# Optimization experiments

Hardware: AMD Instinct MI355X
Metric: run time of the kernel (lower is better)

## Reference

```python
import jax, jax.numpy as jnp
import numpy as np

TEMPERATURE = 0.02
EPS = 1e-10
TOPK = 10


def setup_inputs() -> dict:
    key = jax.random.key(0)
    k1, k2 = jax.random.split(key)
    B = 8192
    sim_matrix = jax.random.normal(k1, (B, B), dtype=jnp.float32)
    pids = jax.random.randint(k2, (B,), 0, 1000, dtype=jnp.int64)
    return {"sim_matrix": sim_matrix, "pids": pids}


def reference(sim_matrix, pids):
    B = sim_matrix.shape[0]
    k = min(TOPK, B)

    # Entropy of the T->I matching distribution per row (matches torch exactly:
    # softmax over dim=1, then -sum p*log(p+eps)).
    probs = jax.nn.softmax(sim_matrix / TEMPERATURE, axis=1)  # [B, B]
    entropy = -jnp.sum(probs * jnp.log(probs + EPS), axis=1)  # [B]
    max_entropy = np.float32(np.log(B + EPS))
    normalized_entropy = entropy / max_entropy  # [B]

    # Vectorized top-k rank agreement between T->I rows and I->T rows
    # (replaces the original per-sample Python loop with set intersection;
    # top-k indices are unique, so counting pairwise equality == |set A & set B|).
    _, top_t2i = jax.lax.top_k(sim_matrix, k)      # [B, k]
    _, top_i2t = jax.lax.top_k(sim_matrix.T, k)    # [B, k]
    overlap = jnp.sum(
        top_t2i[:, :, None] == top_i2t[:, None, :], axis=(1, 2)
    )  # [B]
    rank_agreement = overlap.astype(sim_matrix.dtype) / k  # [B]

    uncertainty = (1.0 - rank_agreement) * 0.5 + normalized_entropy * 0.5
    return uncertainty, normalized_entropy
```

## Files before the change

### kernel.cpp

```cpp
#include <hip/hip_runtime.h>
#include <hip/hip_bf16.h>
#include <math.h>

constexpr int BB = 8192;
constexpr float INV_MAX_ENT = 1.0f / 9.010913347279288f;

#define CAS_STEP(tvk, tik)                                  \
  if (_cv > tvk) {                                          \
    float _fv = tvk; tvk = _cv; _cv = _fv;                  \
    int _fi = tik; tik = _ci; _ci = _fi;                    \
  }

#define INS10(vv, ii)                                       \
  if ((vv) > tv9) {                                         \
    float _cv = (vv);                                       \
    int _ci = (ii);                                         \
    CAS_STEP(tv0, ti0) CAS_STEP(tv1, ti1)                   \
    CAS_STEP(tv2, ti2) CAS_STEP(tv3, ti3)                   \
    CAS_STEP(tv4, ti4) CAS_STEP(tv5, ti5)                   \
    CAS_STEP(tv6, ti6) CAS_STEP(tv7, ti7)                   \
    CAS_STEP(tv8, ti8) CAS_STEP(tv9, ti9)                   \
  }

#define DECL10                                              \
  float tv0 = -INFINITY, tv1 = -INFINITY, tv2 = -INFINITY,  \
        tv3 = -INFINITY, tv4 = -INFINITY, tv5 = -INFINITY,  \
        tv6 = -INFINITY, tv7 = -INFINITY, tv8 = -INFINITY,  \
        tv9 = -INFINITY;                                    \
  int ti0 = -1, ti1 = -1, ti2 = -1, ti3 = -1, ti4 = -1,     \
      ti5 = -1, ti6 = -1, ti7 = -1, ti8 = -1, ti9 = -1;

#define POP_HEAD                                            \
  tv0 = tv1; ti0 = ti1; tv1 = tv2; ti1 = ti2;               \
  tv2 = tv3; ti2 = ti3; tv3 = tv4; ti3 = ti4;               \
  tv4 = tv5; ti4 = ti5; tv5 = tv6; ti5 = ti6;               \
  tv6 = tv7; ti6 = ti7; tv7 = tv8; ti7 = ti8;               \
  tv8 = tv9; ti8 = ti9; tv9 = -INFINITY; ti9 = -1;

__global__ __launch_bounds__(256) void rows_kernel(const float* __restrict__ sim,
                                                   float* __restrict__ out,
                                                   int* __restrict__ row_top) {
  const int lane = threadIdx.x & 63;
  const int wid = threadIdx.x >> 6;
  const int row = blockIdx.x * 4 + wid;

  const float4* __restrict__ r4 =
      reinterpret_cast<const float4*>(sim + (size_t)row * BB);

  DECL10;
  float m = -1e30f, S = 0.0f, W = 0.0f;

#pragma unroll 4
  for (int j4 = 0; j4 < 32; ++j4) {
    const int f = lane + (j4 << 6);
    float4 q = r4[f];

    float mx4 = fmaxf(fmaxf(q.x, q.y), fmaxf(q.z, q.w));
    if (mx4 > tv9) {
      const int base = f << 2;
      INS10(q.x, base + 0);
      INS10(q.y, base + 1);
      INS10(q.z, base + 2);
      INS10(q.w, base + 3);
    }

    float t0 = 50.0f * q.x, t1 = 50.0f * q.y, t2 = 50.0f * q.z, t3 = 50.0f * q.w;
    float bm = fmaxf(fmaxf(t0, t1), fmaxf(t2, t3));
    float mn = fmaxf(m, bm);
    float r = __expf(m - mn);
    float d0 = t0 - mn, d1 = t1 - mn, d2 = t2 - mn, d3 = t3 - mn;
    float e0 = __expf(d0), e1 = __expf(d1), e2 = __expf(d2), e3 = __expf(d3);
    W = fmaf(m - mn, S, W) * r + (d0 * e0 + d1 * e1 + d2 * e2 + d3 * e3);
    S = fmaf(S, r, (e0 + e1) + (e2 + e3));
    m = mn;
  }

#pragma unroll
  for (int off = 32; off; off >>= 1) {
    float m2 = __shfl_xor(m, off);
    float S2 = __shfl_xor(S, off);
    float W2 = __shfl_xor(W, off);
    float mn = fmaxf(m, m2);
    float ra = __expf(m - mn);
    float rb = __expf(m2 - mn);
    W = fmaf(m - mn, S, W) * ra + fmaf(m2 - mn, S2, W2) * rb;
    S = S * ra + S2 * rb;
    m = mn;
  }
  if (lane == 0) {
    out[BB + row] = (__logf(S) - W / S) * INV_MAX_ENT;
  }

#pragma unroll 1
  for (int kk = 0; kk < 10; ++kk) {
    float v = tv0;
    int i = ti0;
#pragma unroll
    for (int off = 32; off; off >>= 1) {
      float ov = __shfl_xor(v, off);
      int oi = __shfl_xor(i, off);
      if (ov > v || (ov == v && oi < i)) { v = ov; i = oi; }
    }
    if (lane == 0) row_top[kk * BB + row] = i;
    if (ti0 == i) { POP_HEAD }
  }
}

__global__ __launch_bounds__(256) void cols_partial_kernel(const float* __restrict__ sim,
                                                           float* __restrict__ pv,
                                                           int* __restrict__ pi,
                                                           int CH) {
  const int col = blockIdx.x * 256 + threadIdx.x;
  const int r0 = blockIdx.y * CH;

  DECL10;

  const float* __restrict__ p = sim + (size_t)r0 * BB + col;

  for (int rr = 0; rr < CH; rr += 8) {
    float v0 = p[0 * BB];
    float v1 = p[1 * BB];
    float v2 = p[2 * BB];
    float v3 = p[3 * BB];
    float v4 = p[4 * BB];
    float v5 = p[5 * BB];
    float v6 = p[6 * BB];
    float v7 = p[7 * BB];
    p += (size_t)8 * BB;
    float mx = fmaxf(fmaxf(fmaxf(v0, v1), fmaxf(v2, v3)),
                     fmaxf(fmaxf(v4, v5), fmaxf(v6, v7)));
    if (mx > tv9) {
      INS10(v0, r0 + rr + 0);
      INS10(v1, r0 + rr + 1);
      INS10(v2, r0 + rr + 2);
      INS10(v3, r0 + rr + 3);
      INS10(v4, r0 + rr + 4);
      INS10(v5, r0 + rr + 5);
      INS10(v6, r0 + rr + 6);
      INS10(v7, r0 + rr + 7);
    }
  }

  float* __restrict__ pvb = pv + (size_t)blockIdx.y * 10 * BB + col;
  int* __restrict__ pib = pi + (size_t)blockIdx.y * 10 * BB + col;
  pvb[0 * BB] = tv0;  pib[0 * BB] = ti0;
  pvb[1 * BB] = tv1;  pib[1 * BB] = ti1;
  pvb[2 * BB] = tv2;  pib[2 * BB] = ti2;
  pvb[3 * BB] = tv3;  pib[3 * BB] = ti3;
  pvb[4 * BB] = tv4;  pib[4 * BB] = ti4;
  pvb[5 * BB] = tv5;  pib[5 * BB] = ti5;
  pvb[6 * BB] = tv6;  pib[6 * BB] = ti6;
  pvb[7 * BB] = tv7;  pib[7 * BB] = ti7;
  pvb[8 * BB] = tv8;  pib[8 * BB] = ti8;
  pvb[9 * BB] = tv9;  pib[9 * BB] = ti9;
}

__global__ __launch_bounds__(256) void merge_kernel(const float* __restrict__ pv,
                                                    const int* __restrict__ pi,
                                                    const int* __restrict__ row_top,
                                                    float* __restrict__ out,
                                                    int nch) {
  const int c = blockIdx.x * 256 + threadIdx.x;

  DECL10;

  for (int ch = 0; ch < nch; ++ch) {
    const float* __restrict__ pvb = pv + (size_t)ch * 10 * BB + c;
    const int* __restrict__ pib = pi + (size_t)ch * 10 * BB + c;
#pragma unroll
    for (int j = 0; j < 10; ++j) {
      float vj = pvb[j * BB];
      if (!(vj > tv9)) break;
      int idj = pib[j * BB];
      INS10(vj, idj);
    }
  }

  int cnt = 0;
#pragma unroll
  for (int kk = 0; kk < 10; ++kk) {
    int rt = row_top[kk * BB + c];
    cnt += (rt == ti0) + (rt == ti1) + (rt == ti2) + (rt == ti3) + (rt == ti4) +
           (rt == ti5) + (rt == ti6) + (rt == ti7) + (rt == ti8) + (rt == ti9);
  }
  float ne = out[BB + c];
  float ra = (float)cnt * 0.1f;
  out[c] = (1.0f - ra) * 0.5f + 0.5f * ne;
}

extern "C" void kernel_launch(void* const* d_in, const int* in_sizes, int n_in,
                              void* d_out, int out_size, void* d_ws, size_t ws_size,
                              hipStream_t stream) {
  const float* sim = (const float*)d_in[0];
  float* out = (float*)d_out;

  int nch = 64;
  while (nch > 1) {
    size_t need = (size_t)BB * 10 * 4 + (size_t)nch * BB * 10 * 8;
    if (need <= ws_size) break;
    nch >>= 1;
  }
  int* row_top = (int*)d_ws;
  float* pv = (float*)((char*)d_ws + (size_t)BB * 10 * 4);
  int* pi = (int*)((char*)pv + (size_t)nch * BB * 10 * 4);

  rows_kernel<<<BB / 4, 256, 0, stream>>>(sim, out, row_top);
  dim3 gb(BB / 256, nch);
  cols_partial_kernel<<<gb, 256, 0, stream>>>(sim, pv, pi, BB / nch);
  merge_kernel<<<BB / 256, 256, 0, stream>>>(pv, pi, row_top, out, nch);
}
```

Baseline: 656.9 us.

## Parallelize top-k merge with one wavefront per column and shuffle selection

The merge kernel now gives each column a whole 64-lane wavefront instead of a single thread. Each lane loads one chunk's partial top-10 list, and ten rounds of wave-wide shuffle argmax pick the global top-10. Each winner is then matched against the row's top-k indices, held one per lane. This replaces a serial per-thread loop over all chunks, which ran on only 32 blocks, with a 2048-block launch. The cost is strided, poorly coalesced loads of the partial arrays, since each lane reads a different chunk, plus more shuffle work.

Result: faster. 545.1 us (-17.0%).

```diff
diff --git a/kernel.cpp b/kernel.cpp
--- a/kernel.cpp
+++ b/kernel.cpp
@@ -160,32 +160,53 @@
                                                     const int* __restrict__ row_top,
                                                     float* __restrict__ out,
                                                     int nch) {
-  const int c = blockIdx.x * 256 + threadIdx.x;
+  const int lane = threadIdx.x & 63;
+  const int wid = threadIdx.x >> 6;
+  const int c = blockIdx.x * 4 + wid;
 
   DECL10;
 
-  for (int ch = 0; ch < nch; ++ch) {
-    const float* __restrict__ pvb = pv + (size_t)ch * 10 * BB + c;
-    const int* __restrict__ pib = pi + (size_t)ch * 10 * BB + c;
-#pragma unroll
-    for (int j = 0; j < 10; ++j) {
-      float vj = pvb[j * BB];
-      if (!(vj > tv9)) break;
-      int idj = pib[j * BB];
-      INS10(vj, idj);
-    }
-  }
+  if (lane < nch) {
+    const float* __restrict__ pvb = pv + (size_t)lane * 10 * BB + c;
+    const int* __restrict__ pib = pi + (size_t)lane * 10 * BB + c;
+    tv0 = pvb[0 * BB];  ti0 = pib[0 * BB];
+    tv1 = pvb[1 * BB];  ti1 = pib[1 * BB];
+    tv2 = pvb[2 * BB];  ti2 = pib[2 * BB];
+    tv3 = pvb[3 * BB];  ti3 = pib[3 * BB];
+    tv4 = pvb[4 * BB];  ti4 = pib[4 * BB];
+    tv5 = pvb[5 * BB];  ti5 = pib[5 * BB];
+    tv6 = pvb[6 * BB];  ti6 = pib[6 * BB];
+    tv7 = pvb[7 * BB];  ti7 = pib[7 * BB];
+    tv8 = pvb[8 * BB];  ti8 = pib[8 * BB];
+    tv9 = pvb[9 * BB];  ti9 = pib[9 * BB];
+  }
+
+  int rt = -1000000;
+  if (lane < 10) rt = row_top[lane * BB + c];
 
   int cnt = 0;
-#pragma unroll
+#pragma unroll 1
   for (int kk = 0; kk < 10; ++kk) {
-    int rt = row_top[kk * BB + c];
-    cnt += (rt == ti0) + (rt == ti1) + (rt == ti2) + (rt == ti3) + (rt == ti4) +
-           (rt == ti5) + (rt == ti6) + (rt == ti7) + (rt == ti8) + (rt == ti9);
-  }
-  float ne = out[BB + c];
-  float ra = (float)cnt * 0.1f;
-  out[c] = (1.0f - ra) * 0.5f + 0.5f * ne;
+    float v = tv0;
+    int i = ti0;
+#pragma unroll
+    for (int off = 32; off; off >>= 1) {
+      float ov = __shfl_xor(v, off);
+      int oi = __shfl_xor(i, off);
+      if (ov > v || (ov == v && oi < i)) { v = ov; i = oi; }
+    }
+    cnt += (rt == i) ? 1 : 0;
+    if (ti0 == i) { POP_HEAD }
+  }
+
+#pragma unroll
+  for (int off = 32; off; off >>= 1) cnt += __shfl_xor(cnt, off);
+
+  if (lane == 0) {
+    float ne = out[BB + c];
+    float ra = (float)cnt * 0.1f;
+    out[c] = (1.0f - ra) * 0.5f + 0.5f * ne;
+  }
 }
 
 extern "C" void kernel_launch(void* const* d_in, const int* in_sizes, int n_in,
@@ -207,5 +228,5 @@
   rows_kernel<<<BB / 4, 256, 0, stream>>>(sim, out, row_top);
   dim3 gb(BB / 256, nch);
   cols_partial_kernel<<<gb, 256, 0, stream>>>(sim, pv, pi, BB / nch);
-  merge_kernel<<<BB / 256, 256, 0, stream>>>(pv, pi, row_top, out, nch);
-}
+  merge_kernel<<<BB / 4, 256, 0, stream>>>(pv, pi, row_top, out, nch);
+}
```
